# Optimization experiments

Measured on AMD Instinct MI355X. Metric: run time of the kernel, lower is better.

## Reference

```python
import jax, jax.numpy as jnp
import numpy as np

TOPK, NUM_CLASSES, ALPHA, BETA = 13, 80, 1.0, 6.0
IOU_EPS = 1e-7


def _cxcywh_to_xyxy(b):
    cx, cy, w, h = b[..., 0], b[..., 1], b[..., 2], b[..., 3]
    return cx - w / 2, cy - h / 2, cx + w / 2, cy + h / 2


def _pairwise_iou(pd, gt):
    # pd: [B,A,4] cxcywh, gt: [B,G,4] cxcywh -> iou [B,A,G]
    p1x, p1y, p2x, p2y = _cxcywh_to_xyxy(pd)
    g1x, g1y, g2x, g2y = _cxcywh_to_xyxy(gt)
    ix1 = jnp.maximum(p1x[:, :, None], g1x[:, None, :])
    iy1 = jnp.maximum(p1y[:, :, None], g1y[:, None, :])
    ix2 = jnp.minimum(p2x[:, :, None], g2x[:, None, :])
    iy2 = jnp.minimum(p2y[:, :, None], g2y[:, None, :])
    inter = jnp.clip(ix2 - ix1, 0) * jnp.clip(iy2 - iy1, 0)
    area_p = (p2x - p1x) * (p2y - p1y)  # [B,A]
    area_g = (g2x - g1x) * (g2y - g1y)  # [B,G]
    union = area_p[:, :, None] + area_g[:, None, :] - inter + IOU_EPS
    return inter / union


def setup_inputs() -> dict:
    key = jax.random.key(0)
    ks = jax.random.split(key, 8)
    B, A, G, C = 32, 8400, 64, 80
    img = 640.0
    pd_scores = jax.random.normal(ks[0], (B, A, C), dtype=jnp.float32)
    pd_cxy = jax.random.uniform(ks[1], (B, A, 2)) * img
    pd_wh = jax.random.uniform(ks[2], (B, A, 2)) * 115.0 + 5.0
    pd_bboxes = jnp.concatenate([pd_cxy, pd_wh], axis=-1).astype(jnp.float32)
    anc_points = (jax.random.uniform(ks[3], (A, 2)) * img).astype(jnp.float32)
    gt_labels = jax.random.randint(ks[4], (B, G, 1), 0, C, dtype=jnp.int32)
    gt_cxy = jax.random.uniform(ks[5], (B, G, 2)) * img
    gt_wh = jax.random.uniform(ks[6], (B, G, 2)) * 115.0 + 5.0
    gt_bboxes = jnp.concatenate([gt_cxy, gt_wh], axis=-1).astype(jnp.float32)
    mask_gt = jax.random.uniform(ks[7], (B, G, 1)) < 0.7  # bool
    return {"pd_scores": pd_scores, "pd_bboxes": pd_bboxes, "anc_points": anc_points,
            "gt_labels": gt_labels, "gt_bboxes": gt_bboxes, "mask_gt": mask_gt}


def reference(pd_scores, pd_bboxes, anc_points, gt_labels, gt_bboxes, mask_gt):
    B, A, C = pd_scores.shape
    G = gt_bboxes.shape[1]
    valid = mask_gt[..., 0].astype(bool)          # [B,G]
    labels = gt_labels[..., 0].astype(jnp.int32)  # [B,G]

    overlaps = _pairwise_iou(pd_bboxes, gt_bboxes)                 # [B,A,G]
    onehot_gt = jax.nn.one_hot(labels, C, dtype=pd_scores.dtype)   # [B,G,C]
    score_gt = jnp.einsum('bac,bgc->bag', pd_scores, onehot_gt)    # gather score at gt class
    metrics = jax.nn.sigmoid(score_gt) ** ALPHA * overlaps ** BETA  # [B,A,G], >= 0
    metrics = jnp.where(valid[:, None, :], metrics, -1.0)          # invalid gt -> sentinel

    # top-k anchors per gt (dim over anchors)
    _, topk_idx = jax.lax.top_k(jnp.swapaxes(metrics, 1, 2), TOPK)  # [B,G,k]
    b_ix = jnp.arange(B)[:, None, None]
    g_ix = jnp.arange(G)[None, :, None]
    cand = jnp.zeros((B, A, G), dtype=bool).at[b_ix, topk_idx, g_ix].set(True)
    cand = cand & valid[:, None, :]

    # (last such gt under ties, matching sequential overwrite order);
    # otherwise the first candidate gt keeps the anchor.
    anchor_max = metrics.max(axis=-1)                               # [B,A]
    is_max_cand = (metrics >= anchor_max[..., None]) & cand         # [B,A,G]
    has_max = is_max_cand.any(axis=-1)
    last_max = (G - 1) - jnp.argmax(is_max_cand[:, :, ::-1].astype(jnp.int32), axis=-1)
    first_cand = jnp.argmax(cand.astype(jnp.int32), axis=-1)
    assigned = jnp.where(has_max, last_max, first_cand)             # [B,A]
    fg = cand.any(axis=-1)                                          # [B,A] bool

    asg_label = jnp.take_along_axis(labels, assigned, axis=1)                   # [B,A]
    asg_bbox = jnp.take_along_axis(gt_bboxes, assigned[:, :, None], axis=1)     # [B,A,4]
    asg_iou = jnp.take_along_axis(overlaps, assigned[:, :, None], axis=2)[..., 0]  # [B,A]

    oh = jax.nn.one_hot(asg_label, C, dtype=pd_scores.dtype)
    fgf = fg.astype(pd_scores.dtype)
    target_labels = oh * fgf[..., None]
    target_bboxes = asg_bbox * fgf[..., None]
    target_scores = oh * (asg_iou * fgf)[..., None]
    return target_labels, target_bboxes, target_scores, fg
```

## Files before the change

kernel.cpp:

```cpp
#include <hip/hip_runtime.h>

#define NB 32
#define NA 8400
#define NG 64
#define NC 80
#define NK 13
#define TILE0 64
#define NT0 132

#define OFF_LBL  0
#define OFF_BBOX 21504000
#define OFF_SCR  22579200
#define OFF_FG   44083200

#define WS_PART_SZ  (32ull*64*132*13*8)
#define WS_MASK_SZ  (32ull*8400*8)
#define WS_AMAX_SZ  (32ull*8400*4)
#define WS_MAXB_SZ  (32ull*8400*8)
#define WS_NEEDED   (WS_PART_SZ + WS_MASK_SZ + WS_AMAX_SZ + WS_MAXB_SZ)

__device__ __forceinline__ float sigmoid_f(float x) {
    return 1.0f / (1.0f + expf(-x));
}

__device__ __forceinline__ float iou_corners(
    float px1, float py1, float px2, float py2, float ap,
    float gx1, float gy1, float gx2, float gy2, float ag)
{
    float ix1 = fmaxf(px1, gx1), iy1 = fmaxf(py1, gy1);
    float ix2 = fminf(px2, gx2), iy2 = fminf(py2, gy2);
    float inter = fmaxf(ix2 - ix1, 0.0f) * fmaxf(iy2 - iy1, 0.0f);
    return inter / (ap + ag - inter + 1e-7f);
}

__global__ __launch_bounds__(256) void metrics_kernel(
    const float* __restrict__ pd_scores,
    const float* __restrict__ pd_bboxes,
    const int* __restrict__ gt_labels,
    const float* __restrict__ gt_bboxes,
    const int* __restrict__ mask_gt,
    float2* __restrict__ partials,
    float* __restrict__ amax_arr,
    unsigned long long* __restrict__ cmask,
    unsigned long long* __restrict__ maxbits)
{
    const int b   = blockIdx.y;
    const int til = blockIdx.x;
    const int a0  = til * TILE0;
    const int tid = threadIdx.x;
    const int an  = min(TILE0, NA - a0);

    __shared__ float s_sc[TILE0 * 81];
    __shared__ float s_pb[TILE0 * 5];
    __shared__ float s_gb[NG * 5];
    __shared__ float s_pm[4][TILE0];
    __shared__ int   s_lab[NG];
    __shared__ int   s_val[NG];

    const float* sbase = pd_scores + ((size_t)b * NA + a0) * NC;
    for (int i4 = tid; i4 < an * 20; i4 += 256) {
        const float4 v = reinterpret_cast<const float4*>(sbase)[i4];
        const int al = i4 / 20;
        const int c  = (i4 % 20) * 4;
        float* d = &s_sc[al * 81 + c];
        d[0] = sigmoid_f(v.x); d[1] = sigmoid_f(v.y);
        d[2] = sigmoid_f(v.z); d[3] = sigmoid_f(v.w);
    }
    if (tid < TILE0) {
        float px1 = 0, py1 = 0, px2 = 0, py2 = 0;
        if (tid < an) {
            const float4 pb = *reinterpret_cast<const float4*>(pd_bboxes + ((size_t)b * NA + a0 + tid) * 4);
            px1 = pb.x - pb.z * 0.5f; py1 = pb.y - pb.w * 0.5f;
            px2 = pb.x + pb.z * 0.5f; py2 = pb.y + pb.w * 0.5f;
        }
        s_pb[tid * 5 + 0] = px1; s_pb[tid * 5 + 1] = py1;
        s_pb[tid * 5 + 2] = px2; s_pb[tid * 5 + 3] = py2;
        s_pb[tid * 5 + 4] = (px2 - px1) * (py2 - py1);
    }
    if (tid >= 64 && tid < 64 + NG) {
        const int g = tid - 64;
        const float4 gb = *reinterpret_cast<const float4*>(gt_bboxes + ((size_t)b * NG + g) * 4);
        const float gx1 = gb.x - gb.z * 0.5f, gy1 = gb.y - gb.w * 0.5f;
        const float gx2 = gb.x + gb.z * 0.5f, gy2 = gb.y + gb.w * 0.5f;
        s_gb[g * 5 + 0] = gx1; s_gb[g * 5 + 1] = gy1;
        s_gb[g * 5 + 2] = gx2; s_gb[g * 5 + 3] = gy2;
        s_gb[g * 5 + 4] = (gx2 - gx1) * (gy2 - gy1);
        s_lab[g] = gt_labels[b * NG + g];
        s_val[g] = mask_gt[b * NG + g];
    }
    __syncthreads();

    const int lane = tid & 63;
    const int wgrp = tid >> 6;
    const float px1 = s_pb[lane * 5 + 0], py1 = s_pb[lane * 5 + 1];
    const float px2 = s_pb[lane * 5 + 2], py2 = s_pb[lane * 5 + 3];
    const float ap  = s_pb[lane * 5 + 4];
    float pm = -1.0f;

    #pragma unroll 4
    for (int gg = 0; gg < 16; ++gg) {
        const int g = gg * 4 + wgrp;
        float m = -1.0f;
        if (lane < an && s_val[g]) {
            const float iou = iou_corners(px1, py1, px2, py2, ap,
                                          s_gb[g*5+0], s_gb[g*5+1], s_gb[g*5+2], s_gb[g*5+3], s_gb[g*5+4]);
            const float i2 = iou * iou;
            m = s_sc[lane * 81 + s_lab[g]] * (i2 * i2 * i2);
        }
        pm = fmaxf(pm, m);

        const unsigned long long pos = __ballot(m > 0.0f);
        const unsigned long long zer = __ballot(m == 0.0f);
        const int n = __popcll(pos);
        int slot = -1;
        if (m > 0.0f) {
            int r = 0;
            unsigned long long rem = pos;
            while (rem) {
                const int j = __ffsll(rem) - 1;
                rem &= rem - 1;
                const float vj = __shfl(m, j);
                r += (vj > m || (vj == m && j < lane)) ? 1 : 0;
            }
            if (r < NK) slot = r;
        } else if (m == 0.0f && n < NK) {
            const int p = __popcll(zer & ((1ull << lane) - 1ull));
            if (p < NK - n) slot = n + p;
        }
        if (slot >= 0) {
            float2 e; e.x = m; e.y = __int_as_float(a0 + lane);
            partials[(((size_t)(b * NG + g)) * NT0 + til) * NK + slot] = e;
        }
    }

    s_pm[wgrp][lane] = pm;
    __syncthreads();
    if (tid < an) {
        const float am = fmaxf(fmaxf(s_pm[0][tid], s_pm[1][tid]),
                               fmaxf(s_pm[2][tid], s_pm[3][tid]));
        amax_arr[(size_t)b * NA + a0 + tid] = am;
        cmask[(size_t)b * NA + a0 + tid]   = 0ull;
        maxbits[(size_t)b * NA + a0 + tid] = 0ull;
    }
}

__global__ __launch_bounds__(256) void merge_kernel(
    const float2* __restrict__ partials,
    const float* __restrict__ amax_arr,
    const int* __restrict__ mask_gt,
    unsigned long long* __restrict__ cmask,
    unsigned long long* __restrict__ maxbits)
{
    const int g = blockIdx.x;
    const int b = blockIdx.y;
    const int tid = threadIdx.x;

    if (mask_gt[b * NG + g] == 0) return;

    const float2* __restrict__ row = partials + ((size_t)(b * NG + g)) * NT0 * NK;

    float v[NK]; int ix[NK];
    #pragma unroll
    for (int k = 0; k < NK; ++k) { v[k] = -3.0f; ix[k] = 0x7fffffff; }

    for (int i = tid; i < NT0 * NK; i += 256) {
        const float2 e = row[i];
        float m = e.x;
        int   a = __float_as_int(e.y);
        if (m > v[NK-1]) {
            #pragma unroll
            for (int k = 0; k < NK; ++k) {
                if (m > v[k]) {
                    const float tv = v[k]; v[k] = m;  m = tv;
                    const int   ti = ix[k]; ix[k] = a; a = ti;
                }
            }
        }
    }

    __shared__ float s_wv[4];
    __shared__ int   s_wi[4];
    __shared__ int   s_sel[NK];
    __shared__ float s_selv[NK];

    for (int r = 0; r < NK; ++r) {
        float bv = v[0]; int bi = ix[0];
        #pragma unroll
        for (int off = 32; off; off >>= 1) {
            const float ov = __shfl_xor(bv, off);
            const int   oi = __shfl_xor(bi, off);
            if (ov > bv || (ov == bv && oi < bi)) { bv = ov; bi = oi; }
        }
        if ((tid & 63) == 0) { s_wv[tid >> 6] = bv; s_wi[tid >> 6] = bi; }
        __syncthreads();
        bv = s_wv[0]; bi = s_wi[0];
        #pragma unroll
        for (int w = 1; w < 4; ++w) {
            if (s_wv[w] > bv || (s_wv[w] == bv && s_wi[w] < bi)) { bv = s_wv[w]; bi = s_wi[w]; }
        }
        if (tid == 0) { s_sel[r] = bi; s_selv[r] = bv; }
        if (v[0] == bv && ix[0] == bi) {
            #pragma unroll
            for (int k = 0; k < NK - 1; ++k) { v[k] = v[k+1]; ix[k] = ix[k+1]; }
            v[NK-1] = -3.0f; ix[NK-1] = 0x7fffffff;
        }
        __syncthreads();
    }

    if (tid < NK) {
        const int a = s_sel[tid];
        atomicOr(&cmask[(size_t)b * NA + a], 1ull << g);
        if (s_selv[tid] >= amax_arr[(size_t)b * NA + a]) {
            atomicOr(&maxbits[(size_t)b * NA + a], 1ull << g);
        }
    }
}

__global__ __launch_bounds__(256) void assign_kernel(
    const float* __restrict__ pd_bboxes,
    const int* __restrict__ gt_labels,
    const float* __restrict__ gt_bboxes,
    const unsigned long long* __restrict__ cmask,
    const unsigned long long* __restrict__ maxbits,
    float* __restrict__ out)
{
    const int b = blockIdx.y;
    const int a0 = blockIdx.x * 256;
    const int tid = threadIdx.x;
    const int a = a0 + tid;
    const bool active = a < NA;

    __shared__ float s_gb[NG * 5];
    __shared__ float s_graw[NG][4];
    __shared__ int   s_lab[NG];
    __shared__ int   s_albl[256];
    __shared__ float s_aiou[256];

    if (tid < NG) {
        const float4 gb = *reinterpret_cast<const float4*>(gt_bboxes + ((size_t)b * NG + tid) * 4);
        s_graw[tid][0] = gb.x; s_graw[tid][1] = gb.y; s_graw[tid][2] = gb.z; s_graw[tid][3] = gb.w;
        const float gx1 = gb.x - gb.z * 0.5f, gy1 = gb.y - gb.w * 0.5f;
        const float gx2 = gb.x + gb.z * 0.5f, gy2 = gb.y + gb.w * 0.5f;
        s_gb[tid * 5 + 0] = gx1; s_gb[tid * 5 + 1] = gy1;
        s_gb[tid * 5 + 2] = gx2; s_gb[tid * 5 + 3] = gy2;
        s_gb[tid * 5 + 4] = (gx2 - gx1) * (gy2 - gy1);
        s_lab[tid] = gt_labels[b * NG + tid];
    }
    __syncthreads();

    unsigned long long cand = 0ull, maxb = 0ull;
    if (active) {
        cand = cmask[(size_t)b * NA + a];
        maxb = maxbits[(size_t)b * NA + a];
    }
    const bool fg = (cand != 0ull);

    int assigned = 0;
    float aiou = 0.0f;
    if (fg) {
        assigned = maxb ? (63 - __clzll(maxb)) : (__ffsll(cand) - 1);
        const float4 pb = *reinterpret_cast<const float4*>(pd_bboxes + ((size_t)b * NA + a) * 4);
        const float px1 = pb.x - pb.z * 0.5f, py1 = pb.y - pb.w * 0.5f;
        const float px2 = pb.x + pb.z * 0.5f, py2 = pb.y + pb.w * 0.5f;
        const float ap = (px2 - px1) * (py2 - py1);
        aiou = iou_corners(px1, py1, px2, py2, ap,
                           s_gb[assigned*5+0], s_gb[assigned*5+1],
                           s_gb[assigned*5+2], s_gb[assigned*5+3], s_gb[assigned*5+4]);
    }

    s_albl[tid] = fg ? s_lab[assigned] : -1;
    s_aiou[tid] = fg ? aiou : 0.0f;

    if (active) {
        float4 ob = fg ? make_float4(s_graw[assigned][0], s_graw[assigned][1],
                                     s_graw[assigned][2], s_graw[assigned][3])
                       : make_float4(0.f, 0.f, 0.f, 0.f);
        *reinterpret_cast<float4*>(out + OFF_BBOX + ((size_t)b * NA + a) * 4) = ob;
        out[OFF_FG + (size_t)b * NA + a] = fg ? 1.0f : 0.0f;
    }
    __syncthreads();

    const int cnt = min(256, NA - a0);
    float4* __restrict__ lblp = reinterpret_cast<float4*>(out + OFF_LBL + ((size_t)b * NA + a0) * NC);
    float4* __restrict__ scrp = reinterpret_cast<float4*>(out + OFF_SCR + ((size_t)b * NA + a0) * NC);
    for (int i4 = tid; i4 < cnt * 20; i4 += 256) {
        const int al = i4 / 20;
        const int cb = (i4 - al * 20) * 4;
        const int lbl = s_albl[al];
        const float aio = s_aiou[al];
        float4 l4, s4;
        l4.x = (cb + 0 == lbl) ? 1.0f : 0.0f;  s4.x = (cb + 0 == lbl) ? aio : 0.0f;
        l4.y = (cb + 1 == lbl) ? 1.0f : 0.0f;  s4.y = (cb + 1 == lbl) ? aio : 0.0f;
        l4.z = (cb + 2 == lbl) ? 1.0f : 0.0f;  s4.z = (cb + 2 == lbl) ? aio : 0.0f;
        l4.w = (cb + 3 == lbl) ? 1.0f : 0.0f;  s4.w = (cb + 3 == lbl) ? aio : 0.0f;
        lblp[i4] = l4;
        scrp[i4] = s4;
    }
}

__global__ __launch_bounds__(256) void topk_fb(
    const float* __restrict__ pd_scores, const float* __restrict__ pd_bboxes,
    const int* __restrict__ gt_labels, const float* __restrict__ gt_bboxes,
    const int* __restrict__ mask_gt, int* __restrict__ topk_idx)
{
    const int g = blockIdx.x, b = blockIdx.y, tid = threadIdx.x;
    int* outp = topk_idx + (b * NG + g) * NK;
    if (mask_gt[b * NG + g] == 0) { if (tid < NK) outp[tid] = -1; return; }
    __shared__ float sm[NA];
    __shared__ float wv[4]; __shared__ int wi[4];
    const int label = gt_labels[b * NG + g];
    const float4 gb = *reinterpret_cast<const float4*>(gt_bboxes + (size_t)(b * NG + g) * 4);
    const float gx1 = gb.x - gb.z * 0.5f, gy1 = gb.y - gb.w * 0.5f;
    const float gx2 = gb.x + gb.z * 0.5f, gy2 = gb.y + gb.w * 0.5f;
    const float ag = (gx2 - gx1) * (gy2 - gy1);
    for (int a = tid; a < NA; a += 256) {
        const float4 pb = *reinterpret_cast<const float4*>(pd_bboxes + ((size_t)b * NA + a) * 4);
        const float px1 = pb.x - pb.z * 0.5f, py1 = pb.y - pb.w * 0.5f;
        const float px2 = pb.x + pb.z * 0.5f, py2 = pb.y + pb.w * 0.5f;
        const float ap = (px2 - px1) * (py2 - py1);
        const float iou = iou_corners(px1, py1, px2, py2, ap, gx1, gy1, gx2, gy2, ag);
        const float s = pd_scores[((size_t)b * NA + a) * NC + label];
        const float i2 = iou * iou;
        sm[a] = sigmoid_f(s) * (i2 * i2 * i2);
    }
    __syncthreads();
    for (int k = 0; k < NK; ++k) {
        float bv = -3.0f; int bi = 0x7fffffff;
        for (int a = tid; a < NA; a += 256) {
            const float vv = sm[a];
            if (vv > bv || (vv == bv && a < bi)) { bv = vv; bi = a; }
        }
        #pragma unroll
        for (int off = 32; off; off >>= 1) {
            const float ov = __shfl_xor(bv, off); const int oi = __shfl_xor(bi, off);
            if (ov > bv || (ov == bv && oi < bi)) { bv = ov; bi = oi; }
        }
        if ((tid & 63) == 0) { wv[tid >> 6] = bv; wi[tid >> 6] = bi; }
        __syncthreads();
        if (tid == 0) {
            #pragma unroll
            for (int w = 1; w < 4; ++w)
                if (wv[w] > bv || (wv[w] == bv && wi[w] < bi)) { bv = wv[w]; bi = wi[w]; }
            outp[k] = bi; sm[bi] = -2.0f;
        }
        __syncthreads();
    }
}

__global__ __launch_bounds__(256) void assign_fb(
    const float* __restrict__ pd_scores, const float* __restrict__ pd_bboxes,
    const int* __restrict__ gt_labels, const float* __restrict__ gt_bboxes,
    const int* __restrict__ mask_gt, const int* __restrict__ topk_idx,
    float* __restrict__ out)
{
    const int b = blockIdx.y, a0 = blockIdx.x * 256, tid = threadIdx.x;
    __shared__ float s_gx1[NG], s_gy1[NG], s_gx2[NG], s_gy2[NG], s_gar[NG];
    __shared__ float s_graw[NG][4];
    __shared__ int s_lab[NG], s_val[NG], s_tk[NG][NK], s_albl[256];
    __shared__ float s_aiou[256];
    if (tid < NG) {
        const float4 gb = *reinterpret_cast<const float4*>(gt_bboxes + ((size_t)b * NG + tid) * 4);
        s_graw[tid][0] = gb.x; s_graw[tid][1] = gb.y; s_graw[tid][2] = gb.z; s_graw[tid][3] = gb.w;
        const float gx1 = gb.x - gb.z * 0.5f, gy1 = gb.y - gb.w * 0.5f;
        const float gx2 = gb.x + gb.z * 0.5f, gy2 = gb.y + gb.w * 0.5f;
        s_gx1[tid] = gx1; s_gy1[tid] = gy1; s_gx2[tid] = gx2; s_gy2[tid] = gy2;
        s_gar[tid] = (gx2 - gx1) * (gy2 - gy1);
        s_lab[tid] = gt_labels[b * NG + tid];
        s_val[tid] = mask_gt[b * NG + tid];
    }
    for (int i = tid; i < NG * NK; i += 256) s_tk[i / NK][i % NK] = topk_idx[(size_t)b * NG * NK + i];
    __syncthreads();
    const int a = a0 + tid;
    const bool active = a < NA;
    float anchor_max = -1.0f;
    unsigned long long cand = 0ull;
    float px1 = 0, py1 = 0, px2 = 0, py2 = 0, ap = 0;
    const float* srow = pd_scores + ((size_t)b * NA + a) * NC;
    if (active) {
        const float4 pb = *reinterpret_cast<const float4*>(pd_bboxes + ((size_t)b * NA + a) * 4);
        px1 = pb.x - pb.z * 0.5f; py1 = pb.y - pb.w * 0.5f;
        px2 = pb.x + pb.z * 0.5f; py2 = pb.y + pb.w * 0.5f;
        ap = (px2 - px1) * (py2 - py1);
        for (int g = 0; g < NG; ++g) {
            if (!s_val[g]) continue;
            const float iou = iou_corners(px1, py1, px2, py2, ap, s_gx1[g], s_gy1[g], s_gx2[g], s_gy2[g], s_gar[g]);
            const float i2 = iou * iou;
            const float m = sigmoid_f(srow[s_lab[g]]) * (i2 * i2 * i2);
            anchor_max = fmaxf(anchor_max, m);
            bool c = false;
            #pragma unroll
            for (int k = 0; k < NK; ++k) c = c || (s_tk[g][k] == a);
            if (c) cand |= (1ull << g);
        }
    }
    const bool fg = (cand != 0ull);
    int assigned = 0; float aiou = 0.0f;
    if (fg) {
        const int first = __ffsll(cand) - 1;
        int lastg = -1;
        unsigned long long rem = cand;
        while (rem) {
            const int g = __ffsll(rem) - 1; rem &= rem - 1;
            const float iou = iou_corners(px1, py1, px2, py2, ap, s_gx1[g], s_gy1[g], s_gx2[g], s_gy2[g], s_gar[g]);
            const float i2 = iou * iou;
            const float m = sigmoid_f(srow[s_lab[g]]) * (i2 * i2 * i2);
            if (m >= anchor_max) lastg = g;
        }
        assigned = (lastg >= 0) ? lastg : first;
        aiou = iou_corners(px1, py1, px2, py2, ap, s_gx1[assigned], s_gy1[assigned], s_gx2[assigned], s_gy2[assigned], s_gar[assigned]);
    }
    s_albl[tid] = fg ? s_lab[assigned] : -1;
    s_aiou[tid] = fg ? aiou : 0.0f;
    if (active) {
        float4 ob = fg ? make_float4(s_graw[assigned][0], s_graw[assigned][1], s_graw[assigned][2], s_graw[assigned][3])
                       : make_float4(0.f, 0.f, 0.f, 0.f);
        *reinterpret_cast<float4*>(out + OFF_BBOX + ((size_t)b * NA + a) * 4) = ob;
        out[OFF_FG + (size_t)b * NA + a] = fg ? 1.0f : 0.0f;
    }
    __syncthreads();
    const int cnt = min(256, NA - a0);
    for (int i = tid; i < cnt * NC; i += 256) {
        const int al = i / NC, c = i - al * NC;
        const int lbl = s_albl[al];
        const size_t base = ((size_t)b * NA + (a0 + al)) * NC + c;
        out[OFF_LBL + base] = (c == lbl) ? 1.0f : 0.0f;
        out[OFF_SCR + base] = (c == lbl) ? s_aiou[al] : 0.0f;
    }
}

extern "C" void kernel_launch(void* const* d_in, const int* in_sizes, int n_in,
                              void* d_out, int out_size, void* d_ws, size_t ws_size,
                              hipStream_t stream) {
    const float* pd_scores = (const float*)d_in[0];
    const float* pd_bboxes = (const float*)d_in[1];
    const int*   gt_labels = (const int*)d_in[3];
    const float* gt_bboxes = (const float*)d_in[4];
    const int*   mask_gt   = (const int*)d_in[5];
    float* out = (float*)d_out;

    if (ws_size >= WS_NEEDED) {
        float2* partials = (float2*)d_ws;
        unsigned long long* cmask = (unsigned long long*)((char*)d_ws + WS_PART_SZ);
        float* amax_arr = (float*)((char*)d_ws + WS_PART_SZ + WS_MASK_SZ);
        unsigned long long* maxbits = (unsigned long long*)((char*)d_ws + WS_PART_SZ + WS_MASK_SZ + WS_AMAX_SZ);

        dim3 g0(NT0, NB);
        metrics_kernel<<<g0, 256, 0, stream>>>(pd_scores, pd_bboxes, gt_labels, gt_bboxes,
                                               mask_gt, partials, amax_arr, cmask, maxbits);

        dim3 g1(NG, NB);
        merge_kernel<<<g1, 256, 0, stream>>>(partials, amax_arr, mask_gt, cmask, maxbits);

        dim3 g2((NA + 255) / 256, NB);
        assign_kernel<<<g2, 256, 0, stream>>>(pd_bboxes, gt_labels, gt_bboxes, cmask, maxbits, out);
    } else {
        int* topk = (int*)d_ws;
        dim3 g1(NG, NB);
        topk_fb<<<g1, 256, 0, stream>>>(pd_scores, pd_bboxes, gt_labels, gt_bboxes, mask_gt, topk);
        dim3 g2((NA + 255) / 256, NB);
        assign_fb<<<g2, 256, 0, stream>>>(pd_scores, pd_bboxes, gt_labels, gt_bboxes, mask_gt, topk, out);
    }
}
```

Before: 322.6 us.

## Interleave candidate masks, merge one gt per wave, use nontemporal output stores

Measured after the change: 332.5 us. +3.1%, slower.

```diff
diff --git a/kernel.cpp b/kernel.cpp
--- a/kernel.cpp
+++ b/kernel.cpp
@@ -14,10 +14,11 @@
 #define OFF_FG   44083200
 
 #define WS_PART_SZ  (32ull*64*132*13*8)
-#define WS_MASK_SZ  (32ull*8400*8)
+#define WS_MASK_SZ  (32ull*8400*16)
 #define WS_AMAX_SZ  (32ull*8400*4)
-#define WS_MAXB_SZ  (32ull*8400*8)
-#define WS_NEEDED   (WS_PART_SZ + WS_MASK_SZ + WS_AMAX_SZ + WS_MAXB_SZ)
+#define WS_NEEDED   (WS_PART_SZ + WS_MASK_SZ + WS_AMAX_SZ)
+
+typedef float f32x4 __attribute__((ext_vector_type(4)));
 
 __device__ __forceinline__ float sigmoid_f(float x) {
     return 1.0f / (1.0f + expf(-x));
@@ -41,8 +42,7 @@
     const int* __restrict__ mask_gt,
     float2* __restrict__ partials,
     float* __restrict__ amax_arr,
-    unsigned long long* __restrict__ cmask,
-    unsigned long long* __restrict__ maxbits)
+    ulonglong2* __restrict__ masks)
 {
     const int b   = blockIdx.y;
     const int til = blockIdx.x;
@@ -139,8 +139,8 @@
         const float am = fmaxf(fmaxf(s_pm[0][tid], s_pm[1][tid]),
                                fmaxf(s_pm[2][tid], s_pm[3][tid]));
         amax_arr[(size_t)b * NA + a0 + tid] = am;
-        cmask[(size_t)b * NA + a0 + tid]   = 0ull;
-        maxbits[(size_t)b * NA + a0 + tid] = 0ull;
+        ulonglong2 z; z.x = 0ull; z.y = 0ull;
+        masks[(size_t)b * NA + a0 + tid] = z;
     }
 }
 
@@ -148,12 +148,12 @@
     const float2* __restrict__ partials,
     const float* __restrict__ amax_arr,
     const int* __restrict__ mask_gt,
-    unsigned long long* __restrict__ cmask,
-    unsigned long long* __restrict__ maxbits)
-{
-    const int g = blockIdx.x;
-    const int b = blockIdx.y;
-    const int tid = threadIdx.x;
+    ulonglong2* __restrict__ masks)
+{
+    const int b    = blockIdx.y;
+    const int wave = threadIdx.x >> 6;
+    const int lane = threadIdx.x & 63;
+    const int g    = blockIdx.x * 4 + wave;
 
     if (mask_gt[b * NG + g] == 0) return;
 
@@ -163,7 +163,7 @@
     #pragma unroll
     for (int k = 0; k < NK; ++k) { v[k] = -3.0f; ix[k] = 0x7fffffff; }
 
-    for (int i = tid; i < NT0 * NK; i += 256) {
+    for (int i = lane; i < NT0 * NK; i += 64) {
         const float2 e = row[i];
         float m = e.x;
         int   a = __float_as_int(e.y);
@@ -178,11 +178,10 @@
         }
     }
 
-    __shared__ float s_wv[4];
-    __shared__ int   s_wi[4];
-    __shared__ int   s_sel[NK];
-    __shared__ float s_selv[NK];
-
+    float selv = -3.0f;
+    int   seli = 0;
+
+    #pragma unroll
     for (int r = 0; r < NK; ++r) {
         float bv = v[0]; int bi = ix[0];
         #pragma unroll
@@ -191,27 +190,19 @@
             const int   oi = __shfl_xor(bi, off);
             if (ov > bv || (ov == bv && oi < bi)) { bv = ov; bi = oi; }
         }
-        if ((tid & 63) == 0) { s_wv[tid >> 6] = bv; s_wi[tid >> 6] = bi; }
-        __syncthreads();
-        bv = s_wv[0]; bi = s_wi[0];
-        #pragma unroll
-        for (int w = 1; w < 4; ++w) {
-            if (s_wv[w] > bv || (s_wv[w] == bv && s_wi[w] < bi)) { bv = s_wv[w]; bi = s_wi[w]; }
-        }
-        if (tid == 0) { s_sel[r] = bi; s_selv[r] = bv; }
+        if (lane == r) { selv = bv; seli = bi; }
         if (v[0] == bv && ix[0] == bi) {
             #pragma unroll
             for (int k = 0; k < NK - 1; ++k) { v[k] = v[k+1]; ix[k] = ix[k+1]; }
             v[NK-1] = -3.0f; ix[NK-1] = 0x7fffffff;
         }
-        __syncthreads();
-    }
-
-    if (tid < NK) {
-        const int a = s_sel[tid];
-        atomicOr(&cmask[(size_t)b * NA + a], 1ull << g);
-        if (s_selv[tid] >= amax_arr[(size_t)b * NA + a]) {
-            atomicOr(&maxbits[(size_t)b * NA + a], 1ull << g);
+    }
+
+    if (lane < NK) {
+        const size_t idx = (size_t)b * NA + seli;
+        atomicOr(&masks[idx].x, 1ull << g);
+        if (selv >= amax_arr[idx]) {
+            atomicOr(&masks[idx].y, 1ull << g);
         }
     }
 }
@@ -220,8 +211,7 @@
     const float* __restrict__ pd_bboxes,
     const int* __restrict__ gt_labels,
     const float* __restrict__ gt_bboxes,
-    const unsigned long long* __restrict__ cmask,
-    const unsigned long long* __restrict__ maxbits,
+    const ulonglong2* __restrict__ masks,
     float* __restrict__ out)
 {
     const int b = blockIdx.y;
@@ -250,8 +240,8 @@
 
     unsigned long long cand = 0ull, maxb = 0ull;
     if (active) {
-        cand = cmask[(size_t)b * NA + a];
-        maxb = maxbits[(size_t)b * NA + a];
+        const ulonglong2 mv = masks[(size_t)b * NA + a];
+        cand = mv.x; maxb = mv.y;
     }
     const bool fg = (cand != 0ull);
 
@@ -272,29 +262,30 @@
     s_aiou[tid] = fg ? aiou : 0.0f;
 
     if (active) {
-        float4 ob = fg ? make_float4(s_graw[assigned][0], s_graw[assigned][1],
-                                     s_graw[assigned][2], s_graw[assigned][3])
-                       : make_float4(0.f, 0.f, 0.f, 0.f);
-        *reinterpret_cast<float4*>(out + OFF_BBOX + ((size_t)b * NA + a) * 4) = ob;
-        out[OFF_FG + (size_t)b * NA + a] = fg ? 1.0f : 0.0f;
+        f32x4 ob;
+        if (fg) { ob.x = s_graw[assigned][0]; ob.y = s_graw[assigned][1];
+                  ob.z = s_graw[assigned][2]; ob.w = s_graw[assigned][3]; }
+        else    { ob.x = 0.f; ob.y = 0.f; ob.z = 0.f; ob.w = 0.f; }
+        __builtin_nontemporal_store(ob, reinterpret_cast<f32x4*>(out + OFF_BBOX + ((size_t)b * NA + a) * 4));
+        __builtin_nontemporal_store(fg ? 1.0f : 0.0f, out + OFF_FG + (size_t)b * NA + a);
     }
     __syncthreads();
 
     const int cnt = min(256, NA - a0);
-    float4* __restrict__ lblp = reinterpret_cast<float4*>(out + OFF_LBL + ((size_t)b * NA + a0) * NC);
-    float4* __restrict__ scrp = reinterpret_cast<float4*>(out + OFF_SCR + ((size_t)b * NA + a0) * NC);
+    f32x4* __restrict__ lblp = reinterpret_cast<f32x4*>(out + OFF_LBL + ((size_t)b * NA + a0) * NC);
+    f32x4* __restrict__ scrp = reinterpret_cast<f32x4*>(out + OFF_SCR + ((size_t)b * NA + a0) * NC);
     for (int i4 = tid; i4 < cnt * 20; i4 += 256) {
         const int al = i4 / 20;
         const int cb = (i4 - al * 20) * 4;
         const int lbl = s_albl[al];
         const float aio = s_aiou[al];
-        float4 l4, s4;
+        f32x4 l4, s4;
         l4.x = (cb + 0 == lbl) ? 1.0f : 0.0f;  s4.x = (cb + 0 == lbl) ? aio : 0.0f;
         l4.y = (cb + 1 == lbl) ? 1.0f : 0.0f;  s4.y = (cb + 1 == lbl) ? aio : 0.0f;
         l4.z = (cb + 2 == lbl) ? 1.0f : 0.0f;  s4.z = (cb + 2 == lbl) ? aio : 0.0f;
         l4.w = (cb + 3 == lbl) ? 1.0f : 0.0f;  s4.w = (cb + 3 == lbl) ? aio : 0.0f;
-        lblp[i4] = l4;
-        scrp[i4] = s4;
+        __builtin_nontemporal_store(l4, lblp + i4);
+        __builtin_nontemporal_store(s4, scrp + i4);
     }
 }
 
@@ -440,19 +431,18 @@
 
     if (ws_size >= WS_NEEDED) {
         float2* partials = (float2*)d_ws;
-        unsigned long long* cmask = (unsigned long long*)((char*)d_ws + WS_PART_SZ);
+        ulonglong2* masks = (ulonglong2*)((char*)d_ws + WS_PART_SZ);
         float* amax_arr = (float*)((char*)d_ws + WS_PART_SZ + WS_MASK_SZ);
-        unsigned long long* maxbits = (unsigned long long*)((char*)d_ws + WS_PART_SZ + WS_MASK_SZ + WS_AMAX_SZ);
 
         dim3 g0(NT0, NB);
         metrics_kernel<<<g0, 256, 0, stream>>>(pd_scores, pd_bboxes, gt_labels, gt_bboxes,
-                                               mask_gt, partials, amax_arr, cmask, maxbits);
-
-        dim3 g1(NG, NB);
-        merge_kernel<<<g1, 256, 0, stream>>>(partials, amax_arr, mask_gt, cmask, maxbits);
+                                               mask_gt, partials, amax_arr, masks);
+
+        dim3 g1(NG / 4, NB);
+        merge_kernel<<<g1, 256, 0, stream>>>(partials, amax_arr, mask_gt, masks);
 
         dim3 g2((NA + 255) / 256, NB);
-        assign_kernel<<<g2, 256, 0, stream>>>(pd_bboxes, gt_labels, gt_bboxes, cmask, maxbits, out);
+        assign_kernel<<<g2, 256, 0, stream>>>(pd_bboxes, gt_labels, gt_bboxes, masks, out);
     } else {
         int* topk = (int*)d_ws;
         dim3 g1(NG, NB);
```
